# Optimization experiments

Hardware: AMD Instinct MI355X
Metric: run time of the kernel (lower is better)

## Reference

```python
import jax, jax.numpy as jnp
import numpy as np

B, L, H = 2, 2048, 1024
NH, HD = 16, 64  # n_heads, head_size


def setup_inputs() -> dict:
    key = jax.random.key(0)
    ks = jax.random.split(key, 12)
    scale = 1.0 / np.sqrt(H)
    inp = {
        "hidden_states": jax.random.normal(ks[0], (B, L, H), dtype=jnp.float32),
        "tau": jax.random.uniform(ks[1], (B, 1), dtype=jnp.float32) + 0.5,
        "delta": jax.random.normal(ks[2], (B, L), dtype=jnp.float32) * 0.1,
        "Wq": jax.random.normal(ks[3], (H, H), dtype=jnp.float32) * scale,
        "bq": jnp.zeros((H,), dtype=jnp.float32),
        "Wk": jax.random.normal(ks[4], (H, H), dtype=jnp.float32) * scale,
        "bk": jnp.zeros((H,), dtype=jnp.float32),
        "Wv": jax.random.normal(ks[5], (H, H), dtype=jnp.float32) * scale,
        "bv": jnp.zeros((H,), dtype=jnp.float32),
        "Wo": jax.random.normal(ks[6], (H, H), dtype=jnp.float32) * scale,
        "bo": jnp.zeros((H,), dtype=jnp.float32),
    }
    return inp


def _split_heads(x):
    # [B, L, H] -> [B, NH, L, HD]
    return x.reshape(B, L, NH, HD).transpose(0, 2, 1, 3)


def reference(hidden_states, tau, delta, Wq, bq, Wk, bk, Wv, bv, Wo, bo):
    q = _split_heads(hidden_states @ Wq.T + bq)
    k = _split_heads(hidden_states @ Wk.T + bk)
    v = _split_heads(hidden_states @ Wv.T + bv)
    tau_b = tau[:, :, None, None]          # [B,1,1,1]
    delta_b = delta[:, None, None, :]      # [B,1,1,L]
    scores = jnp.einsum('bhqd,bhkd->bhqk', q, k) * tau_b + delta_b
    scores = scores / np.sqrt(HD)
    attn = jax.nn.softmax(scores, axis=-1)  # dropout = identity (eval mode)
    ctx = jnp.einsum('bhqk,bhkd->bhqd', attn, v)
    ctx = ctx.transpose(0, 2, 1, 3).reshape(B, L, H)
    return ctx @ Wo.T + bo
```

## Files before the change

kernel.cpp:

```cpp
#include <hip/hip_runtime.h>

#define B_ 2
#define L_ 2048
#define H_ 1024
#define NH_ 16
#define HD_ 64

using short8 = __attribute__((__ext_vector_type__(8))) short;
using f32x4 = __attribute__((__ext_vector_type__(4))) float;
using f32x16 = __attribute__((__ext_vector_type__(16))) float;
typedef unsigned short u16;
typedef unsigned int u32;

__device__ __forceinline__ u16 f2bf(float f) {
  union { float f; unsigned u; } x{f};
  unsigned u = x.u;
  u = u + 0x7FFFu + ((u >> 16) & 1u);
  return (u16)(u >> 16);
}

__device__ __forceinline__ void gld16(const void* g, void* l) {
  __builtin_amdgcn_global_load_lds(
      (const __attribute__((address_space(1))) void*)g,
      (__attribute__((address_space(3))) void*)l, 16, 0, 0);
}

#define MFMA16(a, b, c) __builtin_amdgcn_mfma_f32_16x16x32_bf16((a), (b), (c), 0, 0, 0)
#define MFMA32(a, b, c) __builtin_amdgcn_mfma_f32_32x32x16_bf16((a), (b), (c), 0, 0, 0)

__global__ void cast_all(const float* __restrict__ hs, const float* __restrict__ Wq,
                         const float* __restrict__ Wk, const float* __restrict__ Wv,
                         const float* __restrict__ Wo, const float* __restrict__ delta,
                         u16* __restrict__ dst, float* __restrict__ dsc) {
  const int t = blockIdx.x * 256 + threadIdx.x;
  const int i = t * 4;
  const float* src;
  int off;
  if (i < 4194304) {
    src = hs; off = i;
  } else {
    const int j = i - 4194304;
    const int w = j >> 20;
    off = j & 1048575;
    src = (w == 0) ? Wq : (w == 1) ? Wk : (w == 2) ? Wv : Wo;
  }
  float4 v = *(const float4*)(src + off);
  *(ushort4*)(dst + i) = make_ushort4(f2bf(v.x), f2bf(v.y), f2bf(v.z), f2bf(v.w));
  if (t < 4096) dsc[t] = delta[t] * 0.18033688011112042f;
}

__global__ __launch_bounds__(512) void gemm_qkv256(
    const u16* __restrict__ A, const u16* __restrict__ W,
    const float* __restrict__ bq, const float* __restrict__ bk, const float* __restrict__ bv,
    const float* __restrict__ tau,
    u16* __restrict__ qg, u16* __restrict__ kg, u16* __restrict__ vTg) {
  __shared__ u16 As[2][256 * 64];
  __shared__ u16 Bs[2][256 * 64];
  const int tid = threadIdx.x;
  const int lane = tid & 63;
  const int wid = tid >> 6;
  const int wr = wid >> 2;
  const int wc = wid & 3;
  const int orig = blockIdx.y * 12 + blockIdx.x;
  const int wg = (orig & 7) * 24 + (orig >> 3);
  const int m0 = (wg & 15) * 256;
  const int n0 = (wg >> 4) * 256;

  const int srow = tid >> 3;
  const int sg = tid & 7;

#define STAGE256(slot, t_)                                                              \
  {                                                                                     \
    const int kt64 = (t_) * 64;                                                         \
    _Pragma("unroll") for (int li = 0; li < 4; li++) {                                  \
      const int row = li * 64 + srow;                                                   \
      const int gsrc = sg ^ (row & 7);                                                  \
      gld16(A + (size_t)(m0 + row) * 1024 + kt64 + gsrc * 8,                            \
            (char*)As[slot] + li * 8192 + wid * 1024 + lane * 16);                      \
      gld16(W + (size_t)(n0 + row) * 1024 + kt64 + gsrc * 8,                            \
            (char*)Bs[slot] + li * 8192 + wid * 1024 + lane * 16);                      \
    }                                                                                   \
  }

  f32x4 acc[8][4] = {};

  STAGE256(0, 0);
  STAGE256(1, 1);

  for (int t = 0; t < 16; t++) {
    if (t >= 1 && t + 1 < 16) STAGE256((t + 1) & 1, t + 1);
    if (t + 1 < 16) {
      asm volatile("s_waitcnt vmcnt(8)" ::: "memory");
    } else {
      asm volatile("s_waitcnt vmcnt(0)" ::: "memory");
    }
    asm volatile("s_barrier" ::: "memory");
    const u16* Ab = As[t & 1];
    const u16* Bb = Bs[t & 1];
    short8 bf[4];
#pragma unroll
    for (int q = 0; q < 4; q++) {
      const int mh = q & 1, ks = q >> 1;
      const int g0 = ks * 4 + (lane >> 4);
      if (mh == 0) {
#pragma unroll
        for (int ni = 0; ni < 4; ni++) {
          const int r = wc * 64 + ni * 16 + (lane & 15);
          bf[ni] = *(const short8*)((const char*)Bb + r * 128 + ((g0 ^ (r & 7)) << 4));
        }
      }
      short8 af[4];
#pragma unroll
      for (int mi = 0; mi < 4; mi++) {
        const int r = wr * 128 + (mh * 4 + mi) * 16 + (lane & 15);
        af[mi] = *(const short8*)((const char*)Ab + r * 128 + ((g0 ^ (r & 7)) << 4));
      }
      __builtin_amdgcn_s_setprio(1);
#pragma unroll
      for (int mi = 0; mi < 4; mi++)
#pragma unroll
        for (int ni = 0; ni < 4; ni++)
          acc[mh * 4 + mi][ni] = MFMA16(af[mi], bf[ni], acc[mh * 4 + mi][ni]);
      __builtin_amdgcn_s_setprio(0);
      asm volatile("s_barrier" ::: "memory");
    }
  }

  const int which = n0 >> 10;
  const int b_blk = m0 >> 11;
  const float scl = (which == 0) ? tau[b_blk] * 0.18033688011112042f : 1.0f;
  const float* bias = which == 0 ? bq : (which == 1 ? bk : bv);
#pragma unroll
  for (int ni = 0; ni < 4; ni++) {
    const int n = n0 + wc * 64 + ni * 16 + (lane & 15);
    const int nn = n & 1023;
    const int h = nn >> 6, d = nn & 63;
    const float bb = bias[nn];
#pragma unroll
    for (int mi = 0; mi < 8; mi++) {
      const int mb = m0 + wr * 128 + mi * 16 + ((lane >> 4) << 2);
      const int b = mb >> 11;
      const int lq = mb & 2047;
      if (which == 2) {
        ushort4 pk = make_ushort4(f2bf(acc[mi][ni][0] + bb), f2bf(acc[mi][ni][1] + bb),
                                  f2bf(acc[mi][ni][2] + bb), f2bf(acc[mi][ni][3] + bb));
        *(ushort4*)&vTg[((size_t)(b * NH_ + h) * HD_ + d) * L_ + lq] = pk;
      } else {
        u16* dst = which == 0 ? qg : kg;
#pragma unroll
        for (int r = 0; r < 4; r++)
          dst[((size_t)(b * NH_ + h) * L_ + lq + r) * HD_ + d] = f2bf((acc[mi][ni][r] + bb) * scl);
      }
    }
  }
}

__global__ __launch_bounds__(512) void attn(
    const u16* __restrict__ qg, const u16* __restrict__ kg, const u16* __restrict__ vTg,
    const float* __restrict__ dsc, u16* __restrict__ ctxg) {
  __shared__ u16 lds[2][8192];
  const int tid = threadIdx.x;
  const int lane = tid & 63;
  const int wv = tid >> 6;
  const int lane31 = lane & 31;
  const int hi = lane >> 5;
  const int orig = blockIdx.x;
  const int wgid = (orig & 7) * 32 + (orig >> 3);
  const int bh = wgid >> 3;
  const int qblk = wgid & 7;
  const int b = bh >> 4;
  const int h = bh & 15;
  const int q0 = qblk * 256 + wv * 32;
  const u16* qb = qg + (size_t)bh * L_ * HD_;
  const u16* kb = kg + (size_t)bh * L_ * HD_;
  const u16* vb = vTg + (size_t)bh * HD_ * L_;
  const float* db = dsc + (size_t)b * L_;

  short8 qf[4];
#pragma unroll
  for (int ks = 0; ks < 4; ks++)
    qf[ks] = *(const short8*)&qb[(size_t)(q0 + lane31) * 64 + ks * 16 + hi * 8];

  union { u32 u[4]; short8 s; } onesu;
  const u32 ow = (lane31 == 0) ? 0x3F803F80u : 0u;
  onesu.u[0] = ow; onesu.u[1] = ow; onesu.u[2] = ow; onesu.u[3] = ow;
  const short8 onesf = onesu.s;

  f32x16 acc[2] = {};
  f32x16 accl = {};
  float mrun = -__builtin_inff();

#define STAGE(bufi, j0)                                                                   \
  {                                                                                       \
    u16* bp = lds[bufi];                                                                  \
    {                                                                                     \
      const int kt = wv >> 2, ks = wv & 3;                                                \
      gld16(kb + (size_t)((j0) + kt * 32 + lane31) * 64 + ks * 16 + hi * 8,               \
            bp + wv * 512 + lane * 8);                                                    \
    }                                                                                     \
    {                                                                                     \
      const int kt = wv >> 2, dt = (wv >> 1) & 1, ks2 = wv & 1;                           \
      gld16(vb + (size_t)(dt * 32 + lane31) * L_ + (j0) + kt * 32 + ks2 * 16 + hi * 8,    \
            bp + (8 + wv) * 512 + lane * 8);                                              \
    }                                                                                     \
  }

  STAGE(0, 0);
  __syncthreads();
  int cur = 0;
  for (int jt = 0; jt < L_ / 64; jt++) {
    const int j0 = jt * 64;
    if (jt + 1 < L_ / 64) STAGE(cur ^ 1, j0 + 64);
    const u16* bp = lds[cur];
#pragma unroll
    for (int kt = 0; kt < 2; kt++) {
      f32x16 s = {};
      __builtin_amdgcn_s_setprio(1);
#pragma unroll
      for (int ks = 0; ks < 4; ks++) {
        short8 kf = *(const short8*)&bp[(kt * 4 + ks) * 512 + lane * 8];
        s = MFMA32(kf, qf[ks], s);
      }
      __builtin_amdgcn_s_setprio(0);
      float sv[16];
#pragma unroll
      for (int g = 0; g < 4; g++) {
        float4 dl = *(const float4*)&db[j0 + kt * 32 + g * 8 + hi * 4];
        sv[g * 4 + 0] = s[g * 4 + 0] + dl.x;
        sv[g * 4 + 1] = s[g * 4 + 1] + dl.y;
        sv[g * 4 + 2] = s[g * 4 + 2] + dl.z;
        sv[g * 4 + 3] = s[g * 4 + 3] + dl.w;
      }
      float t0 = fmaxf(fmaxf(sv[0], sv[1]), fmaxf(sv[2], sv[3]));
      float t1 = fmaxf(fmaxf(sv[4], sv[5]), fmaxf(sv[6], sv[7]));
      float t2 = fmaxf(fmaxf(sv[8], sv[9]), fmaxf(sv[10], sv[11]));
      float t3 = fmaxf(fmaxf(sv[12], sv[13]), fmaxf(sv[14], sv[15]));
      float pmax = fmaxf(fmaxf(t0, t1), fmaxf(t2, t3));
      pmax = fmaxf(pmax, __shfl_xor(pmax, 32));
      if (!__all(pmax - mrun <= 11.5f)) {
        float mnew = fmaxf(mrun, pmax);
        float al = __builtin_amdgcn_exp2f(mrun - mnew);
        mrun = mnew;
        accl[0] *= al;
#pragma unroll
        for (int dt = 0; dt < 2; dt++)
#pragma unroll
          for (int r = 0; r < 16; r++) acc[dt][r] *= al;
      }
      float p[16];
#pragma unroll
      for (int r = 0; r < 16; r++) p[r] = __builtin_amdgcn_exp2f(sv[r] - mrun);
      u32 pk[8];
#pragma unroll
      for (int i = 0; i < 8; i++)
        asm("v_cvt_pk_bf16_f32 %0, %1, %2" : "=v"(pk[i]) : "v"(p[2 * i]), "v"(p[2 * i + 1]));
      asm volatile("v_permlane32_swap_b32 %0, %1" : "+v"(pk[0]), "+v"(pk[2]));
      asm volatile("v_permlane32_swap_b32 %0, %1" : "+v"(pk[1]), "+v"(pk[3]));
      asm volatile("v_permlane32_swap_b32 %0, %1" : "+v"(pk[4]), "+v"(pk[6]));
      asm volatile("v_permlane32_swap_b32 %0, %1" : "+v"(pk[5]), "+v"(pk[7]));
      union U8 { u32 u[4]; short8 s; } f0, f1;
      f0.u[0] = pk[0]; f0.u[1] = pk[1]; f0.u[2] = pk[2]; f0.u[3] = pk[3];
      f1.u[0] = pk[4]; f1.u[1] = pk[5]; f1.u[2] = pk[6]; f1.u[3] = pk[7];
      __builtin_amdgcn_s_setprio(1);
#pragma unroll
      for (int ks2 = 0; ks2 < 2; ks2++) {
        short8 pf = ks2 ? f1.s : f0.s;
#pragma unroll
        for (int dt = 0; dt < 2; dt++) {
          short8 vf = *(const short8*)&bp[(8 + kt * 4 + dt * 2 + ks2) * 512 + lane * 8];
          acc[dt] = MFMA32(vf, pf, acc[dt]);
        }
        accl = MFMA32(onesf, pf, accl);
      }
      __builtin_amdgcn_s_setprio(0);
    }
    __syncthreads();
    cur ^= 1;
  }

  __syncthreads();
  u16* tw = (u16*)lds + wv * 2048;
  const float l0 = accl[0];
  const float l1 = __shfl_xor(l0, 32);
  const float inv = 1.0f / (hi ? l1 : l0);
#pragma unroll
  for (int dt = 0; dt < 2; dt++)
#pragma unroll
    for (int g = 0; g < 4; g++) {
      ushort4 w4 = make_ushort4(f2bf(acc[dt][g * 4 + 0] * inv), f2bf(acc[dt][g * 4 + 1] * inv),
                                f2bf(acc[dt][g * 4 + 2] * inv), f2bf(acc[dt][g * 4 + 3] * inv));
      const int d0 = dt * 32 + g * 8 + hi * 4;
      const int byte = (lane31 * 128 + d0 * 2) ^ ((lane31 & 15) << 3);
      *(ushort4*)((char*)tw + byte) = w4;
    }
  asm volatile("s_waitcnt lgkmcnt(0)" ::: "memory");
  const size_t obase = ((size_t)b * L_ + q0) * 1024 + h * 64;
#pragma unroll
  for (int i = 0; i < 16; i++) {
    const int qr = 2 * i + hi;
    const int byte = (qr * 128 + lane31 * 4) ^ ((qr & 15) << 3);
    const u32 val = *(const u32*)((const char*)tw + byte);
    *(u32*)&ctxg[obase + (size_t)qr * 1024 + lane31 * 2] = val;
  }
}

__global__ __launch_bounds__(256) void gemm_out(
    const u16* __restrict__ A, const u16* __restrict__ W,
    const float* __restrict__ bo, float* __restrict__ out) {
  __shared__ u16 As[128 * 64];
  __shared__ u16 Bs[128 * 64];
  const int tid = threadIdx.x;
  const int lane = tid & 63;
  const int wave = tid >> 6;
  const int wrow = (wave >> 1) * 64;
  const int wcol = (wave & 1) * 64;
  const int m0 = blockIdx.y * 128;
  const int n0 = blockIdx.x * 128;
  const int rr = tid >> 3;
  const int c8 = (tid & 7) * 8;
  f32x4 acc[4][4] = {};
  for (int kt = 0; kt < 1024; kt += 64) {
#pragma unroll
    for (int i = 0; i < 4; i++) {
      gld16(A + (size_t)(m0 + i * 32 + rr) * 1024 + kt + c8, (char*)As + i * 4096 + wave * 1024);
      gld16(W + (size_t)(n0 + i * 32 + rr) * 1024 + kt + c8, (char*)Bs + i * 4096 + wave * 1024);
    }
    __syncthreads();
#pragma unroll
    for (int kc = 0; kc < 2; kc++) {
      const int ko = kc * 32 + (lane >> 4) * 8;
      short8 af[4], bf[4];
#pragma unroll
      for (int mi = 0; mi < 4; mi++)
        af[mi] = *(const short8*)&As[(wrow + mi * 16 + (lane & 15)) * 64 + ko];
#pragma unroll
      for (int ni = 0; ni < 4; ni++)
        bf[ni] = *(const short8*)&Bs[(wcol + ni * 16 + (lane & 15)) * 64 + ko];
#pragma unroll
      for (int mi = 0; mi < 4; mi++)
#pragma unroll
        for (int ni = 0; ni < 4; ni++)
          acc[mi][ni] = MFMA16(af[mi], bf[ni], acc[mi][ni]);
    }
    __syncthreads();
  }
#pragma unroll
  for (int ni = 0; ni < 4; ni++) {
    const int n = n0 + wcol + ni * 16 + (lane & 15);
    const float bb = bo[n];
#pragma unroll
    for (int mi = 0; mi < 4; mi++) {
      const int mb = m0 + wrow + mi * 16 + ((lane >> 4) << 2);
#pragma unroll
      for (int r = 0; r < 4; r++)
        out[(size_t)(mb + r) * 1024 + n] = acc[mi][ni][r] + bb;
    }
  }
}

extern "C" void kernel_launch(void* const* d_in, const int* in_sizes, int n_in,
                              void* d_out, int out_size, void* d_ws, size_t ws_size,
                              hipStream_t stream) {
  const float* hs = (const float*)d_in[0];
  const float* tau = (const float*)d_in[1];
  const float* delta = (const float*)d_in[2];
  const float* Wq = (const float*)d_in[3];
  const float* bq = (const float*)d_in[4];
  const float* Wk = (const float*)d_in[5];
  const float* bk = (const float*)d_in[6];
  const float* Wv = (const float*)d_in[7];
  const float* bv = (const float*)d_in[8];
  const float* Wo = (const float*)d_in[9];
  const float* bo = (const float*)d_in[10];
  float* out = (float*)d_out;

  u16* ws = (u16*)d_ws;
  u16* hsb  = ws;
  u16* wqkv = ws + 4194304;
  u16* wob  = ws + 7340032;
  u16* qg   = ws + 8388608;
  u16* kg   = ws + 12582912;
  u16* vTg  = ws + 16777216;
  u16* ctxg = ws + 20971520;
  float* dsc = (float*)(ws + 25165824);

  cast_all<<<8192, 256, 0, stream>>>(hs, Wq, Wk, Wv, Wo, delta, ws, dsc);

  gemm_qkv256<<<dim3(12, 16), 512, 0, stream>>>(hsb, wqkv, bq, bk, bv, tau, qg, kg, vTg);
  attn<<<256, 512, 0, stream>>>(qg, kg, vTg, dsc, ctxg);
  gemm_out<<<dim3(8, 32), 256, 0, stream>>>(ctxg, wob, bo, out);
}
```

Measured before the change: 150.4 us.

## Triple-buffer K/V tiles and software-pipeline QK^T one tile ahead of softmax

The attention loop now keeps three LDS buffers and prefetches two tiles ahead. It computes the next tile's QK^T MFMAs before running the current tile's softmax and PV MFMAs, so matrix work can overlap the exp/max VALU work. Softmax is also processed over the full 64-key tile at once, with one max reduction and one rescale per 64 keys instead of per 32. The cost is more LDS (48KB) and more live registers for the extra score accumulators, which could reduce occupancy or cause spills.

```diff
diff --git a/kernel.cpp b/kernel.cpp
--- a/kernel.cpp
+++ b/kernel.cpp
@@ -158,7 +158,7 @@
 __global__ __launch_bounds__(512) void attn(
     const u16* __restrict__ qg, const u16* __restrict__ kg, const u16* __restrict__ vTg,
     const float* __restrict__ dsc, u16* __restrict__ ctxg) {
-  __shared__ u16 lds[2][8192];
+  __shared__ u16 lds[3][8192];
   const int tid = threadIdx.x;
   const int lane = tid & 63;
   const int wv = tid >> 6;
@@ -190,9 +190,9 @@
   f32x16 accl = {};
   float mrun = -__builtin_inff();
 
-#define STAGE(bufi, j0)                                                                   \
+#define STAGE(bp_, j0)                                                                    \
   {                                                                                       \
-    u16* bp = lds[bufi];                                                                  \
+    u16* bp = (bp_);                                                                      \
     {                                                                                     \
       const int kt = wv >> 2, ks = wv & 3;                                                \
       gld16(kb + (size_t)((j0) + kt * 32 + lane31) * 64 + ks * 16 + hi * 8,               \
@@ -205,80 +205,103 @@
     }                                                                                     \
   }
 
-  STAGE(0, 0);
+#define QK64(bp_, sA_, sB_)                                                               \
+  {                                                                                       \
+    const u16* bp = (bp_);                                                                \
+    __builtin_amdgcn_s_setprio(1);                                                        \
+    _Pragma("unroll") for (int ks = 0; ks < 4; ks++) {                                    \
+      short8 kf0 = *(const short8*)&bp[(0 * 4 + ks) * 512 + lane * 8];                    \
+      short8 kf1 = *(const short8*)&bp[(1 * 4 + ks) * 512 + lane * 8];                    \
+      sA_ = MFMA32(kf0, qf[ks], sA_);                                                     \
+      sB_ = MFMA32(kf1, qf[ks], sB_);                                                     \
+    }                                                                                     \
+    __builtin_amdgcn_s_setprio(0);                                                        \
+  }
+
+  STAGE(lds[0], 0);
+  STAGE(lds[1], 64);
   __syncthreads();
-  int cur = 0;
-  for (int jt = 0; jt < L_ / 64; jt++) {
-    const int j0 = jt * 64;
-    if (jt + 1 < L_ / 64) STAGE(cur ^ 1, j0 + 64);
-    const u16* bp = lds[cur];
+
+  f32x16 sp0 = {}, sp1 = {};
+  QK64(lds[0], sp0, sp1);
+
+  int cur = 0, nxt = 1, fut = 2;
+  for (int t = 0; t < 32; t++) {
+    const int j0 = t * 64;
+    if (t + 2 < 32) STAGE(lds[fut], j0 + 128);
+    f32x16 sn0 = {}, sn1 = {};
+    if (t + 1 < 32) QK64(lds[nxt], sn0, sn1);
+
+#pragma unroll
+    for (int g = 0; g < 4; g++) {
+      float4 dl0 = *(const float4*)&db[j0 + g * 8 + hi * 4];
+      float4 dl1 = *(const float4*)&db[j0 + 32 + g * 8 + hi * 4];
+      sp0[g * 4 + 0] += dl0.x; sp0[g * 4 + 1] += dl0.y;
+      sp0[g * 4 + 2] += dl0.z; sp0[g * 4 + 3] += dl0.w;
+      sp1[g * 4 + 0] += dl1.x; sp1[g * 4 + 1] += dl1.y;
+      sp1[g * 4 + 2] += dl1.z; sp1[g * 4 + 3] += dl1.w;
+    }
+    float tm[8];
+#pragma unroll
+    for (int r = 0; r < 8; r++) tm[r] = fmaxf(fmaxf(sp0[r], sp0[8 + r]), fmaxf(sp1[r], sp1[8 + r]));
+#pragma unroll
+    for (int r = 0; r < 4; r++) tm[r] = fmaxf(tm[r], tm[4 + r]);
+    float pmax = fmaxf(fmaxf(tm[0], tm[1]), fmaxf(tm[2], tm[3]));
+    pmax = fmaxf(pmax, __shfl_xor(pmax, 32));
+    if (!__all(pmax - mrun <= 11.5f)) {
+      float mnew = fmaxf(mrun, pmax);
+      float al = __builtin_amdgcn_exp2f(mrun - mnew);
+      mrun = mnew;
+      accl[0] *= al;
+#pragma unroll
+      for (int dt = 0; dt < 2; dt++)
+#pragma unroll
+        for (int r = 0; r < 16; r++) acc[dt][r] *= al;
+    }
+#pragma unroll
+    for (int r = 0; r < 16; r++) {
+      sp0[r] = __builtin_amdgcn_exp2f(sp0[r] - mrun);
+      sp1[r] = __builtin_amdgcn_exp2f(sp1[r] - mrun);
+    }
+    u32 pk[16];
+#pragma unroll
+    for (int i = 0; i < 8; i++) {
+      asm("v_cvt_pk_bf16_f32 %0, %1, %2" : "=v"(pk[i]) : "v"(sp0[2 * i]), "v"(sp0[2 * i + 1]));
+      asm("v_cvt_pk_bf16_f32 %0, %1, %2" : "=v"(pk[8 + i]) : "v"(sp1[2 * i]), "v"(sp1[2 * i + 1]));
+    }
 #pragma unroll
     for (int kt = 0; kt < 2; kt++) {
-      f32x16 s = {};
+      asm volatile("v_permlane32_swap_b32 %0, %1" : "+v"(pk[kt * 8 + 0]), "+v"(pk[kt * 8 + 2]));
+      asm volatile("v_permlane32_swap_b32 %0, %1" : "+v"(pk[kt * 8 + 1]), "+v"(pk[kt * 8 + 3]));
+      asm volatile("v_permlane32_swap_b32 %0, %1" : "+v"(pk[kt * 8 + 4]), "+v"(pk[kt * 8 + 6]));
+      asm volatile("v_permlane32_swap_b32 %0, %1" : "+v"(pk[kt * 8 + 5]), "+v"(pk[kt * 8 + 7]));
+    }
+    {
+      const u16* bp = lds[cur];
       __builtin_amdgcn_s_setprio(1);
 #pragma unroll
-      for (int ks = 0; ks < 4; ks++) {
-        short8 kf = *(const short8*)&bp[(kt * 4 + ks) * 512 + lane * 8];
-        s = MFMA32(kf, qf[ks], s);
-      }
+      for (int kt = 0; kt < 2; kt++)
+#pragma unroll
+        for (int ks2 = 0; ks2 < 2; ks2++) {
+          union U8 { u32 u[4]; short8 s; } pf;
+          pf.u[0] = pk[kt * 8 + ks2 * 4 + 0];
+          pf.u[1] = pk[kt * 8 + ks2 * 4 + 1];
+          pf.u[2] = pk[kt * 8 + ks2 * 4 + 2];
+          pf.u[3] = pk[kt * 8 + ks2 * 4 + 3];
+#pragma unroll
+          for (int dt = 0; dt < 2; dt++) {
+            short8 vf = *(const short8*)&bp[(8 + kt * 4 + dt * 2 + ks2) * 512 + lane * 8];
+            acc[dt] = MFMA32(vf, pf.s, acc[dt]);
+          }
+          accl = MFMA32(onesf, pf.s, accl);
+        }
       __builtin_amdgcn_s_setprio(0);
-      float sv[16];
-#pragma unroll
-      for (int g = 0; g < 4; g++) {
-        float4 dl = *(const float4*)&db[j0 + kt * 32 + g * 8 + hi * 4];
-        sv[g * 4 + 0] = s[g * 4 + 0] + dl.x;
-        sv[g * 4 + 1] = s[g * 4 + 1] + dl.y;
-        sv[g * 4 + 2] = s[g * 4 + 2] + dl.z;
-        sv[g * 4 + 3] = s[g * 4 + 3] + dl.w;
-      }
-      float t0 = fmaxf(fmaxf(sv[0], sv[1]), fmaxf(sv[2], sv[3]));
-      float t1 = fmaxf(fmaxf(sv[4], sv[5]), fmaxf(sv[6], sv[7]));
-      float t2 = fmaxf(fmaxf(sv[8], sv[9]), fmaxf(sv[10], sv[11]));
-      float t3 = fmaxf(fmaxf(sv[12], sv[13]), fmaxf(sv[14], sv[15]));
-      float pmax = fmaxf(fmaxf(t0, t1), fmaxf(t2, t3));
-      pmax = fmaxf(pmax, __shfl_xor(pmax, 32));
-      if (!__all(pmax - mrun <= 11.5f)) {
-        float mnew = fmaxf(mrun, pmax);
-        float al = __builtin_amdgcn_exp2f(mrun - mnew);
-        mrun = mnew;
-        accl[0] *= al;
-#pragma unroll
-        for (int dt = 0; dt < 2; dt++)
-#pragma unroll
-          for (int r = 0; r < 16; r++) acc[dt][r] *= al;
-      }
-      float p[16];
-#pragma unroll
-      for (int r = 0; r < 16; r++) p[r] = __builtin_amdgcn_exp2f(sv[r] - mrun);
-      u32 pk[8];
-#pragma unroll
-      for (int i = 0; i < 8; i++)
-        asm("v_cvt_pk_bf16_f32 %0, %1, %2" : "=v"(pk[i]) : "v"(p[2 * i]), "v"(p[2 * i + 1]));
-      asm volatile("v_permlane32_swap_b32 %0, %1" : "+v"(pk[0]), "+v"(pk[2]));
-      asm volatile("v_permlane32_swap_b32 %0, %1" : "+v"(pk[1]), "+v"(pk[3]));
-      asm volatile("v_permlane32_swap_b32 %0, %1" : "+v"(pk[4]), "+v"(pk[6]));
-      asm volatile("v_permlane32_swap_b32 %0, %1" : "+v"(pk[5]), "+v"(pk[7]));
-      union U8 { u32 u[4]; short8 s; } f0, f1;
-      f0.u[0] = pk[0]; f0.u[1] = pk[1]; f0.u[2] = pk[2]; f0.u[3] = pk[3];
-      f1.u[0] = pk[4]; f1.u[1] = pk[5]; f1.u[2] = pk[6]; f1.u[3] = pk[7];
-      __builtin_amdgcn_s_setprio(1);
-#pragma unroll
-      for (int ks2 = 0; ks2 < 2; ks2++) {
-        short8 pf = ks2 ? f1.s : f0.s;
-#pragma unroll
-        for (int dt = 0; dt < 2; dt++) {
-          short8 vf = *(const short8*)&bp[(8 + kt * 4 + dt * 2 + ks2) * 512 + lane * 8];
-          acc[dt] = MFMA32(vf, pf, acc[dt]);
-        }
-        accl = MFMA32(onesf, pf, accl);
-      }
-      __builtin_amdgcn_s_setprio(0);
     }
     __syncthreads();
-    cur ^= 1;
-  }
-
-  __syncthreads();
+    sp0 = sn0; sp1 = sn1;
+    const int tmp = cur; cur = nxt; nxt = fut; fut = tmp;
+  }
+
   u16* tw = (u16*)lds + wv * 2048;
   const float l0 = accl[0];
   const float l1 = __shfl_xor(l0, 32);
```

New measurement: 147.1 us. 2.2% less time.
